# Kernel tuning notes

Hardware: AMD Instinct MI355X
Metric: run time of the kernel (lower is better)

The kernel has to match this reference:

```python
import jax, jax.numpy as jnp
import numpy as np

N_BASIS = 16


def _kan_layer(x, coeffs, centers):
    # x: [b, in], coeffs: [out, in, n], centers: [n]
    mu = jnp.mean(x, axis=0)
    sd = jnp.std(x, axis=0, ddof=1)  # torch.std is unbiased by default
    xn = jnp.clip((x - mu) / (sd + 1e-6), -3.0, 3.0)
    # Gaussian RBF expansion: [b, in, n]
    basis = jnp.exp(-((xn[..., None] - centers) ** 2) / 0.5)
    return jnp.einsum('bin,oin->bo', basis, coeffs)


def setup_inputs() -> dict:
    key = jax.random.key(0)
    ks = jax.random.split(key, 6)
    B, IN, H = 16384, 256, 512
    return {
        'x': jax.random.normal(ks[0], (B, IN), jnp.float32),
        'coeffs1': jax.random.normal(ks[1], (H, IN, N_BASIS), jnp.float32) * 0.1,
        'coeffs2': jax.random.normal(ks[2], (H, H, N_BASIS), jnp.float32) * 0.1,
        'coeffs3': jax.random.normal(ks[3], (1, H, N_BASIS), jnp.float32) * 0.1,
        'skip_w': jax.random.normal(ks[4], (1, IN), jnp.float32) * 0.05,
        'skip_b': jnp.zeros((1,), jnp.float32),
    }


def reference(x, coeffs1, coeffs2, coeffs3, skip_w, skip_b):
    centers = jnp.linspace(-2.0, 2.0, N_BASIS).astype(x.dtype)
    h = jnp.tanh(_kan_layer(x, coeffs1, centers))
    h = jnp.tanh(_kan_layer(h, coeffs2, centers))
    out = _kan_layer(h, coeffs3, centers)[:, 0]  # squeeze(-1)
    skip = (x @ skip_w.T + skip_b)[:, 0]
    return out + skip
```

## Files before the change

kernel.cpp:

```cpp
#include <hip/hip_runtime.h>
#include <cstdint>
#include <cstddef>

typedef __attribute__((ext_vector_type(8))) _Float16 half8;
typedef __attribute__((ext_vector_type(4))) _Float16 half4;
typedef __attribute__((ext_vector_type(4))) float    floatx4;

static constexpr int B_ROWS = 16384;
static constexpr int IN_DIM = 256;
static constexpr int H_DIM  = 512;
static constexpr int NB     = 16;

__device__ __forceinline__ float fast_tanh(float x) {
  float ax = fabsf(x);
  float e  = __expf(2.0f * ax);
  float t  = 1.0f - 2.0f / (e + 1.0f);
  return copysignf(t, x);
}

__device__ __forceinline__ void gld16(const void* g, void* l) {
  __builtin_amdgcn_global_load_lds(
      (const __attribute__((address_space(1))) unsigned int*)g,
      (__attribute__((address_space(3))) unsigned int*)l, 16, 0, 0);
}

__global__ __launch_bounds__(256) void prep_k(const float* __restrict__ c1, _Float16* __restrict__ d1, size_t n41,
                                              const float* __restrict__ c2, _Float16* __restrict__ d2, size_t n42,
                                              const float* __restrict__ X,
                                              float* __restrict__ ps, float* __restrict__ ps2) {
  const int bx = blockIdx.x;
  if (bx < 128) {
    int c     = (bx & 3) * 64 + (threadIdx.x & 63);
    int chunk = threadIdx.x >> 6;
    int seg   = bx >> 2;
    int r0    = seg * 512;
    double s = 0.0, s2 = 0.0;
    for (int r = r0 + chunk; r < r0 + 512; r += 4) {
      float v = X[(size_t)r * IN_DIM + c];
      s += v; s2 += (double)v * (double)v;
    }
    __shared__ float Ls[256], Ls2[256];
    Ls[threadIdx.x] = (float)s; Ls2[threadIdx.x] = (float)s2;
    __syncthreads();
    if (chunk == 0) {
      int cl = threadIdx.x;
      float a  = Ls[cl]  + Ls[cl + 64]  + Ls[cl + 128]  + Ls[cl + 192];
      float b  = Ls2[cl] + Ls2[cl + 64] + Ls2[cl + 128] + Ls2[cl + 192];
      ps [(size_t)seg * IN_DIM + c] = a;
      ps2[(size_t)seg * IN_DIM + c] = b;
    }
  } else {
    size_t tot = n41 + n42;
    int nb_blocks = gridDim.x - 128;
    for (size_t i = (size_t)(bx - 128) * 256 + threadIdx.x; i < tot;
         i += (size_t)nb_blocks * 256) {
      const float4* sp; half4* dp; size_t j;
      if (i < n41) { sp = (const float4*)c1; dp = (half4*)d1; j = i; }
      else         { sp = (const float4*)c2; dp = (half4*)d2; j = i - n41; }
      float4 v = sp[j];
      int nb = (int)((j << 2) & 15);
      half4 r;
      float e0 = -2.f + (float)(nb + 0) * (4.f / 15.f);
      float e1 = -2.f + (float)(nb + 1) * (4.f / 15.f);
      float e2 = -2.f + (float)(nb + 2) * (4.f / 15.f);
      float e3 = -2.f + (float)(nb + 3) * (4.f / 15.f);
      r[0] = (_Float16)(v.x * __expf(-2.f * e0 * e0));
      r[1] = (_Float16)(v.y * __expf(-2.f * e1 * e1));
      r[2] = (_Float16)(v.z * __expf(-2.f * e2 * e2));
      r[3] = (_Float16)(v.w * __expf(-2.f * e3 * e3));
      dp[j] = r;
    }
  }
}

__global__ void stats_final_k(const float* __restrict__ ps,
                              const float* __restrict__ ps2,
                              int segs, int cols, int rows,
                              float* __restrict__ mu, float* __restrict__ isd) {
  int c = blockIdx.x * blockDim.x + threadIdx.x;
  if (c >= cols) return;
  double s = 0.0, s2 = 0.0;
  for (int g = 0; g < segs; g++) { s += ps[(size_t)g * cols + c]; s2 += ps2[(size_t)g * cols + c]; }
  double mean = s / rows;
  double var  = (s2 - s * s / rows) / (rows - 1);
  if (var < 0.0) var = 0.0;
  float sd = (float)sqrt(var);
  mu[c]  = (float)mean;
  isd[c] = 1.0f / (sd + 1e-6f);
}

__global__ __launch_bounds__(256, 2) void kan_gemm_fused(const float* __restrict__ X,
                                                         const float* __restrict__ mu,
                                                         const float* __restrict__ isd,
                                                         const _Float16* __restrict__ Bm,
                                                         float* __restrict__ Hout,
                                                         float* __restrict__ psum,
                                                         float* __restrict__ psum2,
                                                         int C) {
  const int K = C << 4;
  const int steps = K >> 5;
  __shared__ __align__(16) _Float16 As[2][128 * 32];
  __shared__ __align__(16) _Float16 Bs[2][128 * 32];
  __shared__ float Rs1[2][128], Rs2[2][128];
  const int tid  = threadIdx.x;
  const int w = tid >> 6, lane = tid & 63;
  const int wm = w & 1, wn = w >> 1;
  const int lrow = lane & 15, quad = lane >> 4;
  const int row0 = blockIdx.x * 128;
  const int col0 = blockIdx.y * 128;

  const int s_row1 = w * 16 + (lane >> 2);
  const int s_row2 = s_row1 + 64;
  const int s_sl   = lane & 3;
  const int s_seg1 = s_sl ^ ((s_row1 >> 1) & 3);
  const int s_seg2 = s_sl ^ ((s_row2 >> 1) & 3);
  const _Float16* gB1 = Bm + (size_t)(col0 + s_row1) * K + s_seg1 * 8;
  const _Float16* gB2 = Bm + (size_t)(col0 + s_row2) * K + s_seg2 * 8;

  const int erow = tid >> 1, eh = tid & 1;
  const float* xp = X + (size_t)(row0 + erow) * C + eh;

  floatx4 acc[4][4] = {};

  auto expand_store = [&](float v, int ci, int bufi) {
    float xn = fminf(fmaxf((v - mu[ci]) * isd[ci], -3.f), 3.f);
    float Wv = __expf(-2.f * xn * xn - 8.f * xn);
    float g  = __expf((16.f / 15.f) * xn);
    half8 h0, h1;
    float p = Wv;
#pragma unroll
    for (int n = 0; n < 8; n++) { h0[n] = (_Float16)p; p *= g; }
#pragma unroll
    for (int n = 0; n < 8; n++) { h1[n] = (_Float16)p; p *= g; }
    *(half8*)&As[bufi][(size_t)((2 * eh)     * 128 + erow) * 8] = h0;
    *(half8*)&As[bufi][(size_t)((2 * eh + 1) * 128 + erow) * 8] = h1;
  };

  gld16(gB1, &Bs[0][(size_t)tid * 8]);
  gld16(gB2, &Bs[0][(size_t)(tid + 256) * 8]);
  expand_store(xp[0], eh, 0);
  float xv = (steps > 1) ? xp[2] : 0.f;
  __syncthreads();

  for (int k = 0; k < steps; k++) {
    const int buf = k & 1, nb = buf ^ 1;
    if (k + 1 < steps) {
      gld16(gB1 + (size_t)(k + 1) * 32, &Bs[nb][(size_t)tid * 8]);
      gld16(gB2 + (size_t)(k + 1) * 32, &Bs[nb][(size_t)(tid + 256) * 8]);
      expand_store(xv, 2 * (k + 1) + eh, nb);
      if (k + 2 < steps) xv = xp[2 * (k + 2)];
    }
    half8 af[4], bf[4];
#pragma unroll
    for (int t = 0; t < 4; t++) {
      int arow = wm * 64 + t * 16 + lrow;
      af[t] = *(const half8*)&As[buf][(quad * 128 + arow) * 8];
      int brow = wn * 64 + t * 16 + lrow;
      int bchunk = brow * 4 + (quad ^ ((brow >> 1) & 3));
      bf[t] = *(const half8*)&Bs[buf][bchunk * 8];
    }
#pragma unroll
    for (int tm = 0; tm < 4; tm++)
#pragma unroll
      for (int tn = 0; tn < 4; tn++)
        acc[tm][tn] = __builtin_amdgcn_mfma_f32_16x16x32_f16(af[tm], bf[tn], acc[tm][tn], 0, 0, 0);
    __syncthreads();
  }

  float s1[4] = {0.f, 0.f, 0.f, 0.f}, s2v[4] = {0.f, 0.f, 0.f, 0.f};
#pragma unroll
  for (int tm = 0; tm < 4; tm++) {
#pragma unroll
    for (int tn = 0; tn < 4; tn++) {
      int gcol = col0 + wn * 64 + tn * 16 + lrow;
#pragma unroll
      for (int r = 0; r < 4; r++) {
        int grow = row0 + wm * 64 + tm * 16 + quad * 4 + r;
        float v = fast_tanh(acc[tm][tn][r]);
        Hout[(size_t)grow * H_DIM + gcol] = v;
        s1[tn] += v; s2v[tn] += v * v;
      }
    }
  }
#pragma unroll
  for (int tn = 0; tn < 4; tn++) {
    s1[tn]  += __shfl_xor(s1[tn], 16);  s1[tn]  += __shfl_xor(s1[tn], 32);
    s2v[tn] += __shfl_xor(s2v[tn], 16); s2v[tn] += __shfl_xor(s2v[tn], 32);
  }
  if (quad == 0) {
#pragma unroll
    for (int tn = 0; tn < 4; tn++) {
      Rs1[wm][wn * 64 + tn * 16 + lrow] = s1[tn];
      Rs2[wm][wn * 64 + tn * 16 + lrow] = s2v[tn];
    }
  }
  __syncthreads();
  if (tid < 128) {
    psum [(size_t)blockIdx.x * H_DIM + col0 + tid] = Rs1[0][tid] + Rs1[1][tid];
    psum2[(size_t)blockIdx.x * H_DIM + col0 + tid] = Rs2[0][tid] + Rs2[1][tid];
  }
}

__global__ __launch_bounds__(256) void layer3_k(const float* __restrict__ H2,
                                                const float* __restrict__ mu,
                                                const float* __restrict__ isd,
                                                const float* __restrict__ C3,
                                                const float* __restrict__ X,
                                                const float* __restrict__ SW,
                                                const float* __restrict__ SB,
                                                float* __restrict__ OUT) {
  int w = threadIdx.x >> 6, lane = threadIdx.x & 63;
  float Kn[NB];
#pragma unroll
  for (int n = 0; n < NB; n++) {
    float c = -2.f + (float)n * (4.f / 15.f);
    Kn[n] = __expf(-2.f * c * c);
  }
  float sb0 = SB[0];
  int row_base = blockIdx.x * 16 + w * 4;
  for (int r = 0; r < 4; r++) {
    int row = row_base + r;
    float s = 0.f;
#pragma unroll
    for (int j = 0; j < 8; j++) {
      int i = lane + 64 * j;
      float hv = H2[(size_t)row * H_DIM + i];
      float xn = fminf(fmaxf((hv - mu[i]) * isd[i], -3.f), 3.f);
      float Wf = __expf(-2.f * xn * xn - 8.f * xn);
      float gf = __expf((16.f / 15.f) * xn);
      const floatx4* cp = (const floatx4*)(C3 + (size_t)i * NB);
      floatx4 c0 = cp[0], c1 = cp[1], c2 = cp[2], c3 = cp[3];
      float p = Wf;
#pragma unroll
      for (int n = 0; n < 4; n++) { s += p * Kn[n]      * c0[n]; p *= gf; }
#pragma unroll
      for (int n = 0; n < 4; n++) { s += p * Kn[n + 4]  * c1[n]; p *= gf; }
#pragma unroll
      for (int n = 0; n < 4; n++) { s += p * Kn[n + 8]  * c2[n]; p *= gf; }
#pragma unroll
      for (int n = 0; n < 4; n++) { s += p * Kn[n + 12] * c3[n]; p *= gf; }
    }
#pragma unroll
    for (int j = 0; j < 4; j++) {
      int i = lane + 64 * j;
      s += X[(size_t)row * IN_DIM + i] * SW[i];
    }
#pragma unroll
    for (int off = 32; off > 0; off >>= 1) s += __shfl_down(s, off);
    if (lane == 0) OUT[row] = s + sb0;
  }
}

extern "C" void kernel_launch(void* const* d_in, const int* in_sizes, int n_in,
                              void* d_out, int out_size, void* d_ws, size_t ws_size,
                              hipStream_t stream) {
  const float* x  = (const float*)d_in[0];
  const float* c1 = (const float*)d_in[1];
  const float* c2 = (const float*)d_in[2];
  const float* c3 = (const float*)d_in[3];
  const float* sw = (const float*)d_in[4];
  const float* sb = (const float*)d_in[5];
  float* out = (float*)d_out;

  const int B = B_ROWS, IN = IN_DIM, H = H_DIM;

  char* ws = (char*)d_ws;
  size_t off = 0;
  auto alloc = [&](size_t bytes) -> void* {
    void* p = ws + off;
    off += (bytes + 255) & ~(size_t)255;
    return p;
  };
  _Float16* C1h = (_Float16*)alloc((size_t)H * IN * NB * 2);
  _Float16* C2h = (_Float16*)alloc((size_t)H * H  * NB * 2);
  float* H1 = (float*)alloc((size_t)B * H * 4);
  float* H2 = (float*)alloc((size_t)B * H * 4);
  float* ps  = (float*)alloc(128 * 512 * 4);
  float* ps2 = (float*)alloc(128 * 512 * 4);
  float* mu  = (float*)alloc(512 * 4);
  float* isd = (float*)alloc(512 * 4);

  prep_k<<<128 + 1024, 256, 0, stream>>>(c1, C1h, (size_t)H * IN * NB / 4,
                                         c2, C2h, (size_t)H * H * NB / 4,
                                         x, ps, ps2);
  stats_final_k<<<1, 256, 0, stream>>>(ps, ps2, 32, IN, B, mu, isd);

  kan_gemm_fused<<<dim3(B / 128, 4), 256, 0, stream>>>(x, mu, isd, C1h, H1, ps, ps2, IN);
  stats_final_k<<<2, 256, 0, stream>>>(ps, ps2, 128, H, B, mu, isd);

  kan_gemm_fused<<<dim3(B / 128, 4), 256, 0, stream>>>(H1, mu, isd, C2h, H2, ps, ps2, H);
  stats_final_k<<<2, 256, 0, stream>>>(ps, ps2, 128, H, B, mu, isd);

  layer3_k<<<B / 16, 256, 0, stream>>>(H2, mu, isd, c3, x, sw, sb, out);
}
```

Baseline: 494.3 us.

## Pre-tile coefficient matrix into MFMA fragment layout and load B directly to registers

The prep kernel now writes the fp16 scaled coefficients in a k-block-major layout, [K/32][H][32], so each lane's MFMA B fragment is a contiguous 16-byte global load. The GEMM drops the B shared-memory tile and global_load_lds staging and instead double-buffers B fragments in registers, unrolling the k loop by two. This removes the LDS traffic and bank-swizzle work for B, freeing LDS for occupancy. In exchange, each wave loads its B fragments from global/L2 with no reuse across the two M-waves, and register pressure rises.

```diff
diff --git a/kernel.cpp b/kernel.cpp
--- a/kernel.cpp
+++ b/kernel.cpp
@@ -18,14 +18,8 @@
   return copysignf(t, x);
 }
 
-__device__ __forceinline__ void gld16(const void* g, void* l) {
-  __builtin_amdgcn_global_load_lds(
-      (const __attribute__((address_space(1))) unsigned int*)g,
-      (__attribute__((address_space(3))) unsigned int*)l, 16, 0, 0);
-}
-
-__global__ __launch_bounds__(256) void prep_k(const float* __restrict__ c1, _Float16* __restrict__ d1, size_t n41,
-                                              const float* __restrict__ c2, _Float16* __restrict__ d2, size_t n42,
+__global__ __launch_bounds__(256) void prep_k(const float* __restrict__ c1, _Float16* __restrict__ d1,
+                                              const float* __restrict__ c2, _Float16* __restrict__ d2,
                                               const float* __restrict__ X,
                                               float* __restrict__ ps, float* __restrict__ ps2) {
   const int bx = blockIdx.x;
@@ -44,31 +38,37 @@
     __syncthreads();
     if (chunk == 0) {
       int cl = threadIdx.x;
-      float a  = Ls[cl]  + Ls[cl + 64]  + Ls[cl + 128]  + Ls[cl + 192];
-      float b  = Ls2[cl] + Ls2[cl + 64] + Ls2[cl + 128] + Ls2[cl + 192];
-      ps [(size_t)seg * IN_DIM + c] = a;
-      ps2[(size_t)seg * IN_DIM + c] = b;
+      ps [(size_t)seg * IN_DIM + c] = Ls[cl]  + Ls[cl + 64]  + Ls[cl + 128]  + Ls[cl + 192];
+      ps2[(size_t)seg * IN_DIM + c] = Ls2[cl] + Ls2[cl + 64] + Ls2[cl + 128] + Ls2[cl + 192];
     }
   } else {
+    const size_t n41 = (size_t)H_DIM * IN_DIM * NB / 4;
+    const size_t n42 = (size_t)H_DIM * H_DIM * NB / 4;
     size_t tot = n41 + n42;
     int nb_blocks = gridDim.x - 128;
-    for (size_t i = (size_t)(bx - 128) * 256 + threadIdx.x; i < tot;
-         i += (size_t)nb_blocks * 256) {
-      const float4* sp; half4* dp; size_t j;
-      if (i < n41) { sp = (const float4*)c1; dp = (half4*)d1; j = i; }
-      else         { sp = (const float4*)c2; dp = (half4*)d2; j = i - n41; }
+    for (size_t idx = (size_t)(bx - 128) * 256 + threadIdx.x; idx < tot;
+         idx += (size_t)nb_blocks * 256) {
+      const float4* sp; _Float16* dp; size_t j; int C;
+      if (idx < n41) { sp = (const float4*)c1; dp = d1; j = idx;       C = IN_DIM; }
+      else           { sp = (const float4*)c2; dp = d2; j = idx - n41; C = H_DIM;  }
       float4 v = sp[j];
-      int nb = (int)((j << 2) & 15);
+      int perO = C * 4;
+      int o    = (int)(j / perO);
+      int rem  = (int)(j - (size_t)o * perO);
+      int i    = rem >> 2;
+      int n0   = (rem & 3) * 4;
+      int kblk = i >> 1;
+      int ksub = (i & 1) * 16 + n0;
       half4 r;
-      float e0 = -2.f + (float)(nb + 0) * (4.f / 15.f);
-      float e1 = -2.f + (float)(nb + 1) * (4.f / 15.f);
-      float e2 = -2.f + (float)(nb + 2) * (4.f / 15.f);
-      float e3 = -2.f + (float)(nb + 3) * (4.f / 15.f);
+      float e0 = -2.f + (float)(n0 + 0) * (4.f / 15.f);
+      float e1 = -2.f + (float)(n0 + 1) * (4.f / 15.f);
+      float e2 = -2.f + (float)(n0 + 2) * (4.f / 15.f);
+      float e3 = -2.f + (float)(n0 + 3) * (4.f / 15.f);
       r[0] = (_Float16)(v.x * __expf(-2.f * e0 * e0));
       r[1] = (_Float16)(v.y * __expf(-2.f * e1 * e1));
       r[2] = (_Float16)(v.z * __expf(-2.f * e2 * e2));
       r[3] = (_Float16)(v.w * __expf(-2.f * e3 * e3));
-      dp[j] = r;
+      *(half4*)(dp + ((size_t)kblk * H_DIM + o) * 32 + ksub) = r;
     }
   }
 }
@@ -92,15 +92,13 @@
 __global__ __launch_bounds__(256, 2) void kan_gemm_fused(const float* __restrict__ X,
                                                          const float* __restrict__ mu,
                                                          const float* __restrict__ isd,
-                                                         const _Float16* __restrict__ Bm,
+                                                         const _Float16* __restrict__ Bt,
                                                          float* __restrict__ Hout,
                                                          float* __restrict__ psum,
                                                          float* __restrict__ psum2,
                                                          int C) {
-  const int K = C << 4;
-  const int steps = K >> 5;
+  const int steps = C >> 1;
   __shared__ __align__(16) _Float16 As[2][128 * 32];
-  __shared__ __align__(16) _Float16 Bs[2][128 * 32];
   __shared__ float Rs1[2][128], Rs2[2][128];
   const int tid  = threadIdx.x;
   const int w = tid >> 6, lane = tid & 63;
@@ -109,13 +107,7 @@
   const int row0 = blockIdx.x * 128;
   const int col0 = blockIdx.y * 128;
 
-  const int s_row1 = w * 16 + (lane >> 2);
-  const int s_row2 = s_row1 + 64;
-  const int s_sl   = lane & 3;
-  const int s_seg1 = s_sl ^ ((s_row1 >> 1) & 3);
-  const int s_seg2 = s_sl ^ ((s_row2 >> 1) & 3);
-  const _Float16* gB1 = Bm + (size_t)(col0 + s_row1) * K + s_seg1 * 8;
-  const _Float16* gB2 = Bm + (size_t)(col0 + s_row2) * K + s_seg2 * 8;
+  const _Float16* bp = Bt + ((size_t)(col0 + wn * 64 + lrow)) * 32 + quad * 8;
 
   const int erow = tid >> 1, eh = tid & 1;
   const float* xp = X + (size_t)(row0 + erow) * C + eh;
@@ -136,35 +128,38 @@
     *(half8*)&As[bufi][(size_t)((2 * eh + 1) * 128 + erow) * 8] = h1;
   };
 
-  gld16(gB1, &Bs[0][(size_t)tid * 8]);
-  gld16(gB2, &Bs[0][(size_t)(tid + 256) * 8]);
+  half8 bA[4], bB[4];
+  float xv;
+
+#pragma unroll
+  for (int t = 0; t < 4; t++) bA[t] = *(const half8*)(bp + (size_t)t * 512);
   expand_store(xp[0], eh, 0);
-  float xv = (steps > 1) ? xp[2] : 0.f;
+  xv = xp[2];
   __syncthreads();
 
-  for (int k = 0; k < steps; k++) {
-    const int buf = k & 1, nb = buf ^ 1;
+  auto body = [&](int k, half8* cur, half8* nxt, int buf) {
     if (k + 1 < steps) {
-      gld16(gB1 + (size_t)(k + 1) * 32, &Bs[nb][(size_t)tid * 8]);
-      gld16(gB2 + (size_t)(k + 1) * 32, &Bs[nb][(size_t)(tid + 256) * 8]);
-      expand_store(xv, 2 * (k + 1) + eh, nb);
+#pragma unroll
+      for (int t = 0; t < 4; t++)
+        nxt[t] = *(const half8*)(bp + (size_t)(k + 1) * 16384 + (size_t)t * 512);
+      expand_store(xv, 2 * (k + 1) + eh, buf ^ 1);
       if (k + 2 < steps) xv = xp[2 * (k + 2)];
     }
-    half8 af[4], bf[4];
-#pragma unroll
-    for (int t = 0; t < 4; t++) {
-      int arow = wm * 64 + t * 16 + lrow;
-      af[t] = *(const half8*)&As[buf][(quad * 128 + arow) * 8];
-      int brow = wn * 64 + t * 16 + lrow;
-      int bchunk = brow * 4 + (quad ^ ((brow >> 1) & 3));
-      bf[t] = *(const half8*)&Bs[buf][bchunk * 8];
-    }
+    half8 af[4];
+#pragma unroll
+    for (int t = 0; t < 4; t++)
+      af[t] = *(const half8*)&As[buf][(quad * 128 + wm * 64 + t * 16 + lrow) * 8];
 #pragma unroll
     for (int tm = 0; tm < 4; tm++)
 #pragma unroll
       for (int tn = 0; tn < 4; tn++)
-        acc[tm][tn] = __builtin_amdgcn_mfma_f32_16x16x32_f16(af[tm], bf[tn], acc[tm][tn], 0, 0, 0);
+        acc[tm][tn] = __builtin_amdgcn_mfma_f32_16x16x32_f16(af[tm], cur[tn], acc[tm][tn], 0, 0, 0);
     __syncthreads();
+  };
+
+  for (int k = 0; k < steps; k += 2) {
+    body(k,     bA, bB, 0);
+    body(k + 1, bB, bA, 1);
   }
 
   float s1[4] = {0.f, 0.f, 0.f, 0.f}, s2v[4] = {0.f, 0.f, 0.f, 0.f};
@@ -271,8 +266,8 @@
     off += (bytes + 255) & ~(size_t)255;
     return p;
   };
-  _Float16* C1h = (_Float16*)alloc((size_t)H * IN * NB * 2);
-  _Float16* C2h = (_Float16*)alloc((size_t)H * H  * NB * 2);
+  _Float16* Bt1 = (_Float16*)alloc((size_t)H * IN * NB * 2);
+  _Float16* Bt2 = (_Float16*)alloc((size_t)H * H  * NB * 2);
   float* H1 = (float*)alloc((size_t)B * H * 4);
   float* H2 = (float*)alloc((size_t)B * H * 4);
   float* ps  = (float*)alloc(128 * 512 * 4);
@@ -280,15 +275,13 @@
   float* mu  = (float*)alloc(512 * 4);
   float* isd = (float*)alloc(512 * 4);
 
-  prep_k<<<128 + 1024, 256, 0, stream>>>(c1, C1h, (size_t)H * IN * NB / 4,
-                                         c2, C2h, (size_t)H * H * NB / 4,
-                                         x, ps, ps2);
+  prep_k<<<128 + 1024, 256, 0, stream>>>(c1, Bt1, c2, Bt2, x, ps, ps2);
   stats_final_k<<<1, 256, 0, stream>>>(ps, ps2, 32, IN, B, mu, isd);
 
-  kan_gemm_fused<<<dim3(B / 128, 4), 256, 0, stream>>>(x, mu, isd, C1h, H1, ps, ps2, IN);
+  kan_gemm_fused<<<dim3(B / 128, 4), 256, 0, stream>>>(x, mu, isd, Bt1, H1, ps, ps2, IN);
   stats_final_k<<<2, 256, 0, stream>>>(ps, ps2, 128, H, B, mu, isd);
 
-  kan_gemm_fused<<<dim3(B / 128, 4), 256, 0, stream>>>(H1, mu, isd, C2h, H2, ps, ps2, H);
+  kan_gemm_fused<<<dim3(B / 128, 4), 256, 0, stream>>>(H1, mu, isd, Bt2, H2, ps, ps2, H);
   stats_final_k<<<2, 256, 0, stream>>>(ps, ps2, 128, H, B, mu, isd);
 
   layer3_k<<<B / 16, 256, 0, stream>>>(H2, mu, isd, c3, x, sw, sb, out);
```

Result: slower. 536.1 us (+8.5%).

## Load B operand directly to registers, fold stats finalization into consumer kernels

Applied to the files above, without the earlier changes.

The GEMM kernel no longer stages B tiles through LDS with global_load_lds. Each wave now loads its B fragments straight from global memory into registers, double-buffered across 64-wide K super-steps, so only the expanded A tile stays in LDS. The three stats_final_k launches are removed: every GEMM block and layer3 block reduces the partial sums itself into shared mu/isd, in float instead of double. This saves launches and LDS traffic, but adds redundant per-block reduction work, more uncoalesced global B reads, higher register pressure, and some precision risk. layer3 also processes 64 rows per block to amortize its reduction.

```diff
diff --git a/kernel.cpp b/kernel.cpp
--- a/kernel.cpp
+++ b/kernel.cpp
@@ -18,16 +18,10 @@
   return copysignf(t, x);
 }
 
-__device__ __forceinline__ void gld16(const void* g, void* l) {
-  __builtin_amdgcn_global_load_lds(
-      (const __attribute__((address_space(1))) unsigned int*)g,
-      (__attribute__((address_space(3))) unsigned int*)l, 16, 0, 0);
-}
-
-__global__ __launch_bounds__(256) void prep_k(const float* __restrict__ c1, _Float16* __restrict__ d1, size_t n41,
-                                              const float* __restrict__ c2, _Float16* __restrict__ d2, size_t n42,
+__global__ __launch_bounds__(256) void prep_k(const float* __restrict__ c1, _Float16* __restrict__ d1,
+                                              const float* __restrict__ c2, _Float16* __restrict__ d2,
                                               const float* __restrict__ X,
-                                              float* __restrict__ ps, float* __restrict__ ps2) {
+                                              float* __restrict__ psx, float* __restrict__ psx2) {
   const int bx = blockIdx.x;
   if (bx < 128) {
     int c     = (bx & 3) * 64 + (threadIdx.x & 63);
@@ -44,12 +38,12 @@
     __syncthreads();
     if (chunk == 0) {
       int cl = threadIdx.x;
-      float a  = Ls[cl]  + Ls[cl + 64]  + Ls[cl + 128]  + Ls[cl + 192];
-      float b  = Ls2[cl] + Ls2[cl + 64] + Ls2[cl + 128] + Ls2[cl + 192];
-      ps [(size_t)seg * IN_DIM + c] = a;
-      ps2[(size_t)seg * IN_DIM + c] = b;
+      psx [(size_t)seg * IN_DIM + c] = Ls[cl]  + Ls[cl + 64]  + Ls[cl + 128]  + Ls[cl + 192];
+      psx2[(size_t)seg * IN_DIM + c] = Ls2[cl] + Ls2[cl + 64] + Ls2[cl + 128] + Ls2[cl + 192];
     }
   } else {
+    const size_t n41 = (size_t)H_DIM * IN_DIM * NB / 4;
+    const size_t n42 = (size_t)H_DIM * H_DIM * NB / 4;
     size_t tot = n41 + n42;
     int nb_blocks = gridDim.x - 128;
     for (size_t i = (size_t)(bx - 128) * 256 + threadIdx.x; i < tot;
@@ -73,98 +67,108 @@
   }
 }
 
-__global__ void stats_final_k(const float* __restrict__ ps,
-                              const float* __restrict__ ps2,
-                              int segs, int cols, int rows,
-                              float* __restrict__ mu, float* __restrict__ isd) {
-  int c = blockIdx.x * blockDim.x + threadIdx.x;
-  if (c >= cols) return;
-  double s = 0.0, s2 = 0.0;
-  for (int g = 0; g < segs; g++) { s += ps[(size_t)g * cols + c]; s2 += ps2[(size_t)g * cols + c]; }
-  double mean = s / rows;
-  double var  = (s2 - s * s / rows) / (rows - 1);
-  if (var < 0.0) var = 0.0;
-  float sd = (float)sqrt(var);
-  mu[c]  = (float)mean;
-  isd[c] = 1.0f / (sd + 1e-6f);
-}
-
 __global__ __launch_bounds__(256, 2) void kan_gemm_fused(const float* __restrict__ X,
-                                                         const float* __restrict__ mu,
-                                                         const float* __restrict__ isd,
+                                                         const float* __restrict__ psin,
+                                                         const float* __restrict__ psin2,
+                                                         int segs,
                                                          const _Float16* __restrict__ Bm,
                                                          float* __restrict__ Hout,
                                                          float* __restrict__ psum,
                                                          float* __restrict__ psum2,
                                                          int C) {
   const int K = C << 4;
-  const int steps = K >> 5;
-  __shared__ __align__(16) _Float16 As[2][128 * 32];
-  __shared__ __align__(16) _Float16 Bs[2][128 * 32];
+  const int supers = C >> 2;
+  __shared__ __align__(16) _Float16 As[2][128 * 64];
+  __shared__ float muL[512], isdL[512];
   __shared__ float Rs1[2][128], Rs2[2][128];
-  const int tid  = threadIdx.x;
+  const int tid = threadIdx.x;
   const int w = tid >> 6, lane = tid & 63;
   const int wm = w & 1, wn = w >> 1;
   const int lrow = lane & 15, quad = lane >> 4;
-  const int row0 = blockIdx.x * 128;
-  const int col0 = blockIdx.y * 128;
-
-  const int s_row1 = w * 16 + (lane >> 2);
-  const int s_row2 = s_row1 + 64;
-  const int s_sl   = lane & 3;
-  const int s_seg1 = s_sl ^ ((s_row1 >> 1) & 3);
-  const int s_seg2 = s_sl ^ ((s_row2 >> 1) & 3);
-  const _Float16* gB1 = Bm + (size_t)(col0 + s_row1) * K + s_seg1 * 8;
-  const _Float16* gB2 = Bm + (size_t)(col0 + s_row2) * K + s_seg2 * 8;
+  const int row0 = blockIdx.x * 128, col0 = blockIdx.y * 128;
+
+  for (int c = tid; c < C; c += 256) {
+    float s = 0.f, s2 = 0.f;
+    for (int g = 0; g < segs; g++) { s += psin[(size_t)g * C + c]; s2 += psin2[(size_t)g * C + c]; }
+    float mean = s / (float)B_ROWS;
+    float var  = (s2 - s * s / (float)B_ROWS) / (float)(B_ROWS - 1);
+    var = fmaxf(var, 0.f);
+    muL[c]  = mean;
+    isdL[c] = 1.f / (sqrtf(var) + 1e-6f);
+  }
+  __syncthreads();
 
   const int erow = tid >> 1, eh = tid & 1;
   const float* xp = X + (size_t)(row0 + erow) * C + eh;
-
-  floatx4 acc[4][4] = {};
-
-  auto expand_store = [&](float v, int ci, int bufi) {
-    float xn = fminf(fmaxf((v - mu[ci]) * isd[ci], -3.f), 3.f);
+  _Float16* a0[2] = { &As[0][((2 * eh) * 128 + erow) * 8],
+                      &As[1][((2 * eh) * 128 + erow) * 8] };
+  _Float16* a1[2] = { &As[0][((2 * eh + 4) * 128 + erow) * 8],
+                      &As[1][((2 * eh + 4) * 128 + erow) * 8] };
+
+  auto expand2 = [&](float v, int ci, _Float16* dst) {
+    float xn = fminf(fmaxf((v - muL[ci]) * isdL[ci], -3.f), 3.f);
     float Wv = __expf(-2.f * xn * xn - 8.f * xn);
     float g  = __expf((16.f / 15.f) * xn);
-    half8 h0, h1;
-    float p = Wv;
+    half8 h0, h1; float p = Wv;
 #pragma unroll
     for (int n = 0; n < 8; n++) { h0[n] = (_Float16)p; p *= g; }
 #pragma unroll
     for (int n = 0; n < 8; n++) { h1[n] = (_Float16)p; p *= g; }
-    *(half8*)&As[bufi][(size_t)((2 * eh)     * 128 + erow) * 8] = h0;
-    *(half8*)&As[bufi][(size_t)((2 * eh + 1) * 128 + erow) * 8] = h1;
+    *(half8*)dst          = h0;
+    *(half8*)(dst + 1024) = h1;
   };
 
-  gld16(gB1, &Bs[0][(size_t)tid * 8]);
-  gld16(gB2, &Bs[0][(size_t)(tid + 256) * 8]);
-  expand_store(xp[0], eh, 0);
-  float xv = (steps > 1) ? xp[2] : 0.f;
+  const _Float16* bp = Bm + (size_t)(col0 + wn * 64 + lrow) * K + quad * 8;
+
+  floatx4 acc[4][4] = {};
+  half8 bA[8], bB[8];
+
+#pragma unroll
+  for (int t = 0; t < 4; t++) {
+    bA[t]     = *(const half8*)(bp + (size_t)t * 16 * K);
+    bA[4 + t] = *(const half8*)(bp + (size_t)t * 16 * K + 32);
+  }
+  expand2(xp[0], eh, a0[0]);
+  expand2(xp[2], eh + 2, a1[0]);
+  float xv0 = xp[4], xv1 = xp[6];
   __syncthreads();
 
-  for (int k = 0; k < steps; k++) {
-    const int buf = k & 1, nb = buf ^ 1;
-    if (k + 1 < steps) {
-      gld16(gB1 + (size_t)(k + 1) * 32, &Bs[nb][(size_t)tid * 8]);
-      gld16(gB2 + (size_t)(k + 1) * 32, &Bs[nb][(size_t)(tid + 256) * 8]);
-      expand_store(xv, 2 * (k + 1) + eh, nb);
-      if (k + 2 < steps) xv = xp[2 * (k + 2)];
-    }
-    half8 af[4], bf[4];
-#pragma unroll
-    for (int t = 0; t < 4; t++) {
-      int arow = wm * 64 + t * 16 + lrow;
-      af[t] = *(const half8*)&As[buf][(quad * 128 + arow) * 8];
-      int brow = wn * 64 + t * 16 + lrow;
-      int bchunk = brow * 4 + (quad ^ ((brow >> 1) & 3));
-      bf[t] = *(const half8*)&Bs[buf][bchunk * 8];
-    }
+  auto super_body = [&](int k, half8* cur, half8* nxt, int buf) {
+    if (k + 1 < supers) {
+      size_t koff = (size_t)(k + 1) * 64;
+#pragma unroll
+      for (int t = 0; t < 4; t++) {
+        nxt[t]     = *(const half8*)(bp + (size_t)t * 16 * K + koff);
+        nxt[4 + t] = *(const half8*)(bp + (size_t)t * 16 * K + koff + 32);
+      }
+      int fb = 4 * (k + 1);
+      expand2(xv0, fb + eh, a0[buf ^ 1]);
+      expand2(xv1, fb + eh + 2, a1[buf ^ 1]);
+      if (k + 2 < supers) { xv0 = xp[4 * (k + 2)]; xv1 = xp[4 * (k + 2) + 2]; }
+    }
+    half8 af[4];
+#pragma unroll
+    for (int t = 0; t < 4; t++)
+      af[t] = *(const half8*)&As[buf][((quad) * 128 + wm * 64 + t * 16 + lrow) * 8];
 #pragma unroll
     for (int tm = 0; tm < 4; tm++)
 #pragma unroll
       for (int tn = 0; tn < 4; tn++)
-        acc[tm][tn] = __builtin_amdgcn_mfma_f32_16x16x32_f16(af[tm], bf[tn], acc[tm][tn], 0, 0, 0);
+        acc[tm][tn] = __builtin_amdgcn_mfma_f32_16x16x32_f16(af[tm], cur[tn], acc[tm][tn], 0, 0, 0);
+#pragma unroll
+    for (int t = 0; t < 4; t++)
+      af[t] = *(const half8*)&As[buf][((4 + quad) * 128 + wm * 64 + t * 16 + lrow) * 8];
+#pragma unroll
+    for (int tm = 0; tm < 4; tm++)
+#pragma unroll
+      for (int tn = 0; tn < 4; tn++)
+        acc[tm][tn] = __builtin_amdgcn_mfma_f32_16x16x32_f16(af[tm], cur[4 + tn], acc[tm][tn], 0, 0, 0);
     __syncthreads();
+  };
+
+  for (int k = 0; k < supers; k += 2) {
+    super_body(k,     bA, bB, 0);
+    super_body(k + 1, bB, bA, 1);
   }
 
   float s1[4] = {0.f, 0.f, 0.f, 0.f}, s2v[4] = {0.f, 0.f, 0.f, 0.f};
@@ -202,14 +206,27 @@
 }
 
 __global__ __launch_bounds__(256) void layer3_k(const float* __restrict__ H2,
-                                                const float* __restrict__ mu,
-                                                const float* __restrict__ isd,
+                                                const float* __restrict__ psin,
+                                                const float* __restrict__ psin2,
                                                 const float* __restrict__ C3,
                                                 const float* __restrict__ X,
                                                 const float* __restrict__ SW,
                                                 const float* __restrict__ SB,
                                                 float* __restrict__ OUT) {
-  int w = threadIdx.x >> 6, lane = threadIdx.x & 63;
+  __shared__ float muL[H_DIM], isdL[H_DIM];
+  int tid = threadIdx.x;
+  for (int c = tid; c < H_DIM; c += 256) {
+    float s = 0.f, s2 = 0.f;
+    for (int g = 0; g < 128; g++) { s += psin[(size_t)g * H_DIM + c]; s2 += psin2[(size_t)g * H_DIM + c]; }
+    float mean = s / (float)B_ROWS;
+    float var  = (s2 - s * s / (float)B_ROWS) / (float)(B_ROWS - 1);
+    var = fmaxf(var, 0.f);
+    muL[c]  = mean;
+    isdL[c] = 1.f / (sqrtf(var) + 1e-6f);
+  }
+  __syncthreads();
+
+  int w = tid >> 6, lane = tid & 63;
   float Kn[NB];
 #pragma unroll
   for (int n = 0; n < NB; n++) {
@@ -217,15 +234,15 @@
     Kn[n] = __expf(-2.f * c * c);
   }
   float sb0 = SB[0];
-  int row_base = blockIdx.x * 16 + w * 4;
-  for (int r = 0; r < 4; r++) {
+  int row_base = blockIdx.x * 64 + w * 16;
+  for (int r = 0; r < 16; r++) {
     int row = row_base + r;
     float s = 0.f;
 #pragma unroll
     for (int j = 0; j < 8; j++) {
       int i = lane + 64 * j;
       float hv = H2[(size_t)row * H_DIM + i];
-      float xn = fminf(fmaxf((hv - mu[i]) * isd[i], -3.f), 3.f);
+      float xn = fminf(fmaxf((hv - muL[i]) * isdL[i], -3.f), 3.f);
       float Wf = __expf(-2.f * xn * xn - 8.f * xn);
       float gf = __expf((16.f / 15.f) * xn);
       const floatx4* cp = (const floatx4*)(C3 + (size_t)i * NB);
@@ -273,23 +290,20 @@
   };
   _Float16* C1h = (_Float16*)alloc((size_t)H * IN * NB * 2);
   _Float16* C2h = (_Float16*)alloc((size_t)H * H  * NB * 2);
-  float* H1 = (float*)alloc((size_t)B * H * 4);
-  float* H2 = (float*)alloc((size_t)B * H * 4);
-  float* ps  = (float*)alloc(128 * 512 * 4);
-  float* ps2 = (float*)alloc(128 * 512 * 4);
-  float* mu  = (float*)alloc(512 * 4);
-  float* isd = (float*)alloc(512 * 4);
-
-  prep_k<<<128 + 1024, 256, 0, stream>>>(c1, C1h, (size_t)H * IN * NB / 4,
-                                         c2, C2h, (size_t)H * H * NB / 4,
-                                         x, ps, ps2);
-  stats_final_k<<<1, 256, 0, stream>>>(ps, ps2, 32, IN, B, mu, isd);
-
-  kan_gemm_fused<<<dim3(B / 128, 4), 256, 0, stream>>>(x, mu, isd, C1h, H1, ps, ps2, IN);
-  stats_final_k<<<2, 256, 0, stream>>>(ps, ps2, 128, H, B, mu, isd);
-
-  kan_gemm_fused<<<dim3(B / 128, 4), 256, 0, stream>>>(H1, mu, isd, C2h, H2, ps, ps2, H);
-  stats_final_k<<<2, 256, 0, stream>>>(ps, ps2, 128, H, B, mu, isd);
-
-  layer3_k<<<B / 16, 256, 0, stream>>>(H2, mu, isd, c3, x, sw, sb, out);
-}
+  float* H1  = (float*)alloc((size_t)B * H * 4);
+  float* H2  = (float*)alloc((size_t)B * H * 4);
+  float* psx  = (float*)alloc(32 * 256 * 4);
+  float* psx2 = (float*)alloc(32 * 256 * 4);
+  float* psA  = (float*)alloc(128 * 512 * 4);
+  float* psA2 = (float*)alloc(128 * 512 * 4);
+  float* psB  = (float*)alloc(128 * 512 * 4);
+  float* psB2 = (float*)alloc(128 * 512 * 4);
+
+  prep_k<<<128 + 1024, 256, 0, stream>>>(c1, C1h, c2, C2h, x, psx, psx2);
+
+  kan_gemm_fused<<<dim3(B / 128, 4), 256, 0, stream>>>(x, psx, psx2, 32, C1h, H1, psA, psA2, IN);
+
+  kan_gemm_fused<<<dim3(B / 128, 4), 256, 0, stream>>>(H1, psA, psA2, 128, C2h, H2, psB, psB2, H);
+
+  layer3_k<<<B / 64, 256, 0, stream>>>(H2, psB, psB2, c3, x, sw, sb, out);
+}
```

Result: slower. 669.5 us (+35.4%).
